# Performance work log

Hardware: AMD Instinct MI355X
Metric: run time of the kernel (lower is better)

The kernel has to match this reference:

```python
import jax, jax.numpy as jnp
import numpy as np

F = 128; K = 64; SR_CUT = 10.0
NB = 5; NRI = 3; NRA = 2; NRO = 1
N_ATOMS = 10000; N_PAIRS = 320000


def act(x):
    # shifted softplus: softplus(x) - log(2)
    return jax.nn.softplus(x) - jnp.log(2.0).astype(x.dtype)


def residual(x, W1, b1, W2, b2):
    # PhysNet residual: x + dense2(dense1(act(x))) with activation on dense1
    h = act(act(x) @ W1 + b1)
    return x + h @ W2 + b2


def cutoff_fn(D):
    x = D / SR_CUT
    x3 = x * x * x; x4 = x3 * x; x5 = x4 * x
    return jnp.where(x < 1.0, 1.0 - 6.0 * x5 + 15.0 * x4 - 10.0 * x3, 0.0)


def setup_inputs() -> dict:
    key = jax.random.key(0)
    ks = jax.random.split(key, 24)

    def nrm(k, shape, s=0.05):
        return (jax.random.normal(k, shape) * s).astype(jnp.float32)

    inp = {}
    inp["Z"] = jax.random.randint(ks[0], (N_ATOMS,), 1, 95)
    inp["R"] = (jax.random.normal(ks[1], (N_ATOMS, 3)) * 3.0).astype(jnp.float32)
    inp["idx_i"] = jax.random.randint(ks[2], (N_PAIRS,), 0, N_ATOMS)
    inp["idx_j"] = jax.random.randint(ks[3], (N_PAIRS,), 0, N_ATOMS)
    s3 = float(np.sqrt(3.0))
    inp["embeddings"] = jax.random.uniform(ks[4], (95, F), minval=-s3, maxval=s3).astype(jnp.float32)
    inp["rbf_centers"] = jnp.linspace(1.0, float(np.exp(-SR_CUT)), K).astype(jnp.float32)
    width = (0.5 / ((1.0 - float(np.exp(-SR_CUT))) / K)) ** 2
    inp["rbf_widths"] = jnp.full((K,), width, dtype=jnp.float32)
    inp["k2f_W"] = nrm(ks[5], (NB, K, F))
    inp["Wi"] = nrm(ks[6], (NB, F, F)); inp["bi"] = jnp.zeros((NB, F), jnp.float32)
    inp["Wj"] = nrm(ks[7], (NB, F, F)); inp["bj"] = jnp.zeros((NB, F), jnp.float32)
    inp["ri_W1"] = nrm(ks[8], (NB, NRI, F, F)); inp["ri_b1"] = jnp.zeros((NB, NRI, F), jnp.float32)
    inp["ri_W2"] = nrm(ks[9], (NB, NRI, F, F)); inp["ri_b2"] = jnp.zeros((NB, NRI, F), jnp.float32)
    inp["dW"] = nrm(ks[10], (NB, F, F)); inp["db"] = jnp.zeros((NB, F), jnp.float32)
    inp["u"] = jnp.ones((NB, F), jnp.float32)
    inp["ra_W1"] = nrm(ks[11], (NB, NRA, F, F)); inp["ra_b1"] = jnp.zeros((NB, NRA, F), jnp.float32)
    inp["ra_W2"] = nrm(ks[12], (NB, NRA, F, F)); inp["ra_b2"] = jnp.zeros((NB, NRA, F), jnp.float32)
    inp["ro_W1"] = nrm(ks[13], (NB, NRO, F, F)); inp["ro_b1"] = jnp.zeros((NB, NRO, F), jnp.float32)
    inp["ro_W2"] = nrm(ks[14], (NB, NRO, F, F)); inp["ro_b2"] = jnp.zeros((NB, NRO, F), jnp.float32)
    inp["out_W"] = nrm(ks[15], (NB, F, 2))
    inp["Escale"] = jnp.ones((95,), jnp.float32); inp["Eshift"] = jnp.zeros((95,), jnp.float32)
    inp["Qscale"] = jnp.ones((95,), jnp.float32); inp["Qshift"] = jnp.zeros((95,), jnp.float32)
    return inp


def reference(Z, R, idx_i, idx_j, embeddings, rbf_centers, rbf_widths, k2f_W, Wi, bi, Wj, bj,
              ri_W1, ri_b1, ri_W2, ri_b2, dW, db, u, ra_W1, ra_b1, ra_W2, ra_b2,
              ro_W1, ro_b1, ro_W2, ro_b2, out_W, Escale, Eshift, Qscale, Qshift):
    N = R.shape[0]
    # gather-based interatomic distances: gather -> sub -> sumsq -> relu -> sqrt
    dR = R[idx_i] - R[idx_j]                                   # [P,3]
    Dij = jnp.sqrt(jax.nn.relu(jnp.sum(dR * dR, axis=-1)))     # [P]
    # RBF expansion with smooth cutoff
    rbf = cutoff_fn(Dij)[:, None] * jnp.exp(-rbf_widths * (jnp.exp(-Dij)[:, None] - rbf_centers) ** 2)  # [P,K]
    x = embeddings[Z]                                          # [N,F]
    Ea = jnp.zeros((N,), x.dtype)
    Qa = jnp.zeros((N,), x.dtype)
    nhloss = jnp.zeros((), x.dtype)
    last2 = None
    for b in range(NB):
        # --- interaction layer ---
        g = rbf @ k2f_W[b]                                     # [P,F]
        xa = act(x)
        xi = act(xa @ Wi[b] + bi[b])                           # [N,F]
        xj_feat = act(xa @ Wj[b] + bj[b])                      # [N,F]
        msg = g * xj_feat[idx_j]                               # [P,F] gather + modulate
        m = xi + jax.ops.segment_sum(msg, idx_i, num_segments=N)
        for l in range(NRI):
            m = residual(m, ri_W1[b, l], ri_b1[b, l], ri_W2[b, l], ri_b2[b, l])
        m = act(m)
        x = u[b] * x + m @ dW[b] + db[b]
        for l in range(NRA):
            x = residual(x, ra_W1[b, l], ra_b1[b, l], ra_W2[b, l], ra_b2[b, l])
        # --- output block ---
        o = x
        for l in range(NRO):
            o = residual(o, ro_W1[b, l], ro_b1[b, l], ro_W2[b, l], ro_b2[b, l])
        out = act(o) @ out_W[b]                                # [N,2] -> (Ea, Qa)
        Ea = Ea + out[:, 0]
        Qa = Qa + out[:, 1]
        out2 = out * out
        if b > 0:
            nhloss = nhloss + jnp.mean(out2 / (out2 + last2 + 1e-7))
        last2 = out2
    Ea = Escale[Z] * Ea + Eshift[Z]
    Qa = Qscale[Z] * Qa + Qshift[Z]
    return Ea, Qa, Dij, nhloss
```

## Files before the change

### kernel.cpp

```cpp
#include <hip/hip_runtime.h>

typedef __attribute__((ext_vector_type(8))) short bfrag;
typedef __attribute__((ext_vector_type(4))) float ffrag;

__device__ __forceinline__ unsigned short f2b(float f){
  unsigned int u = __float_as_uint(f);
  return (unsigned short)((u + 0x7FFFu + ((u >> 16) & 1u)) >> 16);
}
__device__ __forceinline__ float b2f_lo(unsigned int v){
  return __uint_as_float(v << 16);
}
__device__ __forceinline__ float b2f_hi(unsigned int v){
  return __uint_as_float(v & 0xFFFF0000u);
}
__device__ __forceinline__ float actf(float v){
  float e = __builtin_amdgcn_exp2f(-fabsf(v)*1.44269504088896341f);
  return fmaxf(v, 0.f) + __builtin_amdgcn_logf(1.f + e)*0.69314718055994531f - 0.69314718055994531f;
}

__global__ __launch_bounds__(256) void k_zero(float* p, int n){
  int i = blockIdx.x*256 + threadIdx.x;
  if (i < n) p[i] = 0.f;
}

__global__ __launch_bounds__(256) void k_dij_count(
    const float* __restrict__ R, const int* __restrict__ idx_i, const int* __restrict__ idx_j,
    float* __restrict__ DijF, float* __restrict__ Dout, int* __restrict__ counts, int P){
  int p = blockIdx.x*256 + threadIdx.x;
  if (p >= P) return;
  int i = idx_i[p], j = idx_j[p];
  float dx = R[i*3+0] - R[j*3+0];
  float dy = R[i*3+1] - R[j*3+1];
  float dz = R[i*3+2] - R[j*3+2];
  float D = sqrtf(fmaxf(dx*dx + dy*dy + dz*dz, 0.f));
  DijF[p] = D;
  Dout[p] = D;
  atomicAdd(&counts[i], 1);
}

__global__ __launch_bounds__(1024) void k_scan(const int* __restrict__ counts,
    int* __restrict__ cursor, int N){
  __shared__ int wsum[16];
  int tid = threadIdx.x;
  int CH = (N + 1023) >> 10;
  int base = tid * CH;
  int s = 0;
  for (int i = 0; i < CH; ++i){
    int idx = base + i;
    s += (idx < N) ? counts[idx] : 0;
  }
  int lane = tid & 63, w = tid >> 6;
  int v = s;
  #pragma unroll
  for (int off = 1; off < 64; off <<= 1){
    int t = __shfl_up(v, off, 64);
    if (lane >= off) v += t;
  }
  if (lane == 63) wsum[w] = v;
  __syncthreads();
  if (tid < 16){
    int t = wsum[tid];
    int vv = t;
    #pragma unroll
    for (int off = 1; off < 16; off <<= 1){
      int u = __shfl_up(vv, off, 64);
      if (tid >= off) vv += u;
    }
    wsum[tid] = vv - t;
  }
  __syncthreads();
  int run = (v - s) + wsum[w];
  for (int i = 0; i < CH; ++i){
    int idx = base + i;
    if (idx < N){ cursor[idx] = run; run += counts[idx]; }
  }
}

__global__ __launch_bounds__(256) void k_scatter(const int* __restrict__ idx_i,
    const int* __restrict__ idx_j, const float* __restrict__ DijF,
    int* __restrict__ cursor, int* __restrict__ i_s, int* __restrict__ j_s,
    float* __restrict__ D_s, int P){
  int p = blockIdx.x*256 + threadIdx.x;
  if (p >= P) return;
  int i = idx_i[p];
  int pos = atomicAdd(&cursor[i], 1);
  i_s[pos] = i;
  j_s[pos] = idx_j[p];
  D_s[pos] = DijF[p];
}

__global__ __launch_bounds__(256) void k_rbf(
    const float* __restrict__ D_s, const float* __restrict__ cent, const float* __restrict__ wid,
    unsigned short* __restrict__ rbf_s, int P){
  int gid = blockIdx.x*256 + threadIdx.x;
  if (gid >= P*8) return;
  int t = gid >> 3, kg = gid & 7;
  float D = D_s[t];
  float xc = D * 0.1f;
  float cut = 0.f;
  if (xc < 1.f){
    float x3 = xc*xc*xc, x4 = x3*xc, x5 = x4*xc;
    cut = 1.f - 6.f*x5 + 15.f*x4 - 10.f*x3;
  }
  float eD = __builtin_amdgcn_exp2f(-D*1.44269504088896341f);
  bfrag o;
  #pragma unroll
  for (int i = 0; i < 8; ++i){
    int k = kg*8 + i;
    float tt = eD - cent[k];
    float v = cut * __builtin_amdgcn_exp2f(-wid[k]*tt*tt*1.44269504088896341f);
    o[i] = (short)f2b(v);
  }
  *(bfrag*)(rbf_s + (size_t)gid*8) = o;
}

__global__ __launch_bounds__(256) void k_prepAll(
    const float* __restrict__ riW1, const float* __restrict__ riW2,
    const float* __restrict__ dW,   const float* __restrict__ raW1,
    const float* __restrict__ raW2, const float* __restrict__ roW1,
    const float* __restrict__ roW2, const float* __restrict__ Wi,
    const float* __restrict__ Wj,   const float* __restrict__ k2f,
    const float* __restrict__ outW,
    unsigned short* __restrict__ WBall, unsigned short* __restrict__ k2fP,
    unsigned short* __restrict__ outWB){
  int gid = blockIdx.x*256 + threadIdx.x;
  if (gid < 75*2048){
    int i = gid >> 11, r = gid & 2047;
    const float* S;
    int slot;
    if (i < 15)      { S = riW1 + (size_t)i*16384;      slot = (i/3)*15 + 2*(i%3); }
    else if (i < 30) { int j=i-15; S = riW2 + (size_t)j*16384; slot = (j/3)*15 + 2*(j%3) + 1; }
    else if (i < 35) { int j=i-30; S = dW   + (size_t)j*16384; slot = j*15 + 6; }
    else if (i < 45) { int j=i-35; S = raW1 + (size_t)j*16384; slot = (j/2)*15 + 7 + 2*(j%2); }
    else if (i < 55) { int j=i-45; S = raW2 + (size_t)j*16384; slot = (j/2)*15 + 8 + 2*(j%2); }
    else if (i < 60) { int j=i-55; S = roW1 + (size_t)j*16384; slot = j*15 + 11; }
    else if (i < 65) { int j=i-60; S = roW2 + (size_t)j*16384; slot = j*15 + 12; }
    else if (i < 70) { int j=i-65; S = Wi   + (size_t)j*16384; slot = ((j==0)?4:(j-1))*15 + 13; }
    else             { int j=i-70; S = Wj   + (size_t)j*16384; slot = ((j==0)?4:(j-1))*15 + 14; }
    int fr = r >> 6, l = r & 63;
    int T = fr >> 2, k0 = fr & 3;
    int n = T*16 + (l & 15);
    int kbase = k0*32 + (l >> 4)*8;
    unsigned short* D = WBall + ((size_t)slot*2048 + r)*8;
    ushort4 o0, o1;
    o0.x=f2b(S[(kbase+0)*128+n]); o0.y=f2b(S[(kbase+1)*128+n]);
    o0.z=f2b(S[(kbase+2)*128+n]); o0.w=f2b(S[(kbase+3)*128+n]);
    o1.x=f2b(S[(kbase+4)*128+n]); o1.y=f2b(S[(kbase+5)*128+n]);
    o1.z=f2b(S[(kbase+6)*128+n]); o1.w=f2b(S[(kbase+7)*128+n]);
    ((ushort4*)D)[0]=o0; ((ushort4*)D)[1]=o1;
  } else if (gid < 75*2048 + 5120){
    int g = gid - 75*2048;
    int l = g & 63, fr = (g >> 6) & 15, b = g >> 10;
    int tile = fr >> 1, kh = fr & 1;
    const float* src = k2f + (size_t)b*64*128;
    int n = tile*16 + (l & 15);
    int kbase = kh*32 + (l >> 4)*8;
    ushort4 o0, o1;
    o0.x = f2b(src[(kbase+0)*128+n]); o0.y = f2b(src[(kbase+1)*128+n]);
    o0.z = f2b(src[(kbase+2)*128+n]); o0.w = f2b(src[(kbase+3)*128+n]);
    o1.x = f2b(src[(kbase+4)*128+n]); o1.y = f2b(src[(kbase+5)*128+n]);
    o1.z = f2b(src[(kbase+6)*128+n]); o1.w = f2b(src[(kbase+7)*128+n]);
    ushort4* dst = (ushort4*)(k2fP + (size_t)g*8);
    dst[0] = o0; dst[1] = o1;
  } else if (gid < 75*2048 + 5120 + 1280){
    int g = gid - (75*2048 + 5120);
    int b = g >> 8, r = g & 255;
    int l = r & 63;
    int col = l & 15;
    int k0 = r >> 6;
    int kbase = k0*32 + (l >> 4)*8;
    ushort4 o0 = {0,0,0,0}, o1 = {0,0,0,0};
    if (col < 2){
      const float* S = outW + (size_t)b*256;
      o0.x=f2b(S[(kbase+0)*2+col]); o0.y=f2b(S[(kbase+1)*2+col]);
      o0.z=f2b(S[(kbase+2)*2+col]); o0.w=f2b(S[(kbase+3)*2+col]);
      o1.x=f2b(S[(kbase+4)*2+col]); o1.y=f2b(S[(kbase+5)*2+col]);
      o1.z=f2b(S[(kbase+6)*2+col]); o1.w=f2b(S[(kbase+7)*2+col]);
    }
    unsigned short* D = outWB + ((size_t)b*256 + r)*8;
    ((ushort4*)D)[0]=o0; ((ushort4*)D)[1]=o1;
  }
}

__device__ __forceinline__ void mmtile(const unsigned short* tile,
    const unsigned short* __restrict__ WB, int w, int l, ffrag C[4]){
  int m = l & 15, q = l >> 4;
  bfrag A[4];
  #pragma unroll
  for (int k0 = 0; k0 < 4; ++k0)
    A[k0] = *(const bfrag*)(tile + m*136 + k0*32 + q*8);
  #pragma unroll
  for (int tt = 0; tt < 4; ++tt){
    ffrag c = {0.f,0.f,0.f,0.f};
    const bfrag* bp = (const bfrag*)(WB + (((w*4+tt)*4)*64 + l)*8);
    #pragma unroll
    for (int k0 = 0; k0 < 4; ++k0)
      c = __builtin_amdgcn_mfma_f32_16x16x32_bf16(A[k0], bp[k0*64], c, 0, 0, 0);
    C[tt] = c;
  }
}

__global__ __launch_bounds__(128) void k_phase1m(
    const int* __restrict__ Z, const float* __restrict__ emb,
    const unsigned short* __restrict__ WB45,
    const float* __restrict__ bi0, const float* __restrict__ bj0,
    float* __restrict__ x_g, float* __restrict__ m_g, unsigned short* __restrict__ xjb_g, int N){
  __shared__ unsigned short tile[16*136];
  int tid = threadIdx.x, w = tid >> 6, l = tid & 63;
  int m = l & 15, q = l >> 4, rbase = blockIdx.x*16;
  #pragma unroll
  for (int r = 0; r < 4; ++r){
    int row = rbase + q*4 + r;
    int z = Z[row];
    #pragma unroll
    for (int tt = 0; tt < 4; ++tt){
      int c = (w*4+tt)*16 + m;
      float v = emb[(size_t)z*128 + c];
      x_g[(size_t)row*128 + c] = v;
      tile[(q*4+r)*136 + c] = f2b(actf(v));
    }
  }
  __syncthreads();
  ffrag C[4];
  mmtile(tile, WB45 + 13*16384, w, l, C);
  #pragma unroll
  for (int tt = 0; tt < 4; ++tt){
    int c = (w*4+tt)*16 + m;
    float bb = bi0[c];
    #pragma unroll
    for (int r = 0; r < 4; ++r)
      m_g[(size_t)(rbase + q*4 + r)*128 + c] = actf(C[tt][r] + bb);
  }
  mmtile(tile, WB45 + 14*16384, w, l, C);
  #pragma unroll
  for (int tt = 0; tt < 4; ++tt){
    int c = (w*4+tt)*16 + m;
    float bb = bj0[c];
    #pragma unroll
    for (int r = 0; r < 4; ++r)
      xjb_g[(size_t)(rbase + q*4 + r)*128 + c] = f2b(actf(C[tt][r] + bb));
  }
}

__global__ __launch_bounds__(256) void k_pairmsg2(
    const unsigned short* __restrict__ rbf_s, const unsigned short* __restrict__ k2fP,
    const int* __restrict__ i_s, const int* __restrict__ j_s,
    const unsigned short* __restrict__ xj, float* __restrict__ m_g, int P){
  __shared__ float G[4][16*130];
  int tid = threadIdx.x, w = tid >> 6, l = tid & 63;
  float* Gw = &G[w][0];
  bfrag B[16];
  #pragma unroll
  for (int t = 0; t < 8; ++t){
    #pragma unroll
    for (int kh = 0; kh < 2; ++kh)
      B[t*2+kh] = *(const bfrag*)(k2fP + (size_t)((t*2+kh)*64 + l)*8);
  }
  int wstart = (blockIdx.x*4 + w)*128;
  if (wstart >= P) return;
  int row16 = l & 15, quad = l >> 4;
  float a0 = 0.f, a1 = 0.f;
  int iCur = -1;
  bfrag A0 = *(const bfrag*)(rbf_s + (size_t)(wstart + row16)*64 + quad*8);
  bfrag A1 = *(const bfrag*)(rbf_s + (size_t)(wstart + row16)*64 + 32 + quad*8);
  int4 iv[4], jv[4];
  #pragma unroll
  for (int g = 0; g < 4; ++g){
    iv[g] = *(const int4*)(i_s + wstart + g*4);
    jv[g] = *(const int4*)(j_s + wstart + g*4);
  }
  unsigned int xv[16];
  {
    const int* jp = (const int*)jv;
    #pragma unroll
    for (int k = 0; k < 16; ++k)
      xv[k] = *(const unsigned int*)(xj + (size_t)jp[k]*128 + 2*l);
  }
  #pragma unroll 1
  for (int bi2 = 0; bi2 < 8; ++bi2){
    int bt = wstart + bi2*16;
    const int* ip = (const int*)iv;
    int4 niv[4], njv[4];
    if (bi2 < 7){
      int btn = bt + 16;
      #pragma unroll
      for (int g = 0; g < 4; ++g){
        niv[g] = *(const int4*)(i_s + btn + g*4);
        njv[g] = *(const int4*)(j_s + btn + g*4);
      }
    }
    #pragma unroll
    for (int t = 0; t < 8; ++t){
      ffrag C = {0.f,0.f,0.f,0.f};
      C = __builtin_amdgcn_mfma_f32_16x16x32_bf16(A0, B[t*2],   C, 0, 0, 0);
      C = __builtin_amdgcn_mfma_f32_16x16x32_bf16(A1, B[t*2+1], C, 0, 0, 0);
      #pragma unroll
      for (int r = 0; r < 4; ++r)
        Gw[(quad*4+r)*130 + t*16 + row16] = C[r];
    }
    bfrag nA0, nA1;
    unsigned int nxv[16];
    if (bi2 < 7){
      int btn = bt + 16;
      nA0 = *(const bfrag*)(rbf_s + (size_t)(btn + row16)*64 + quad*8);
      nA1 = *(const bfrag*)(rbf_s + (size_t)(btn + row16)*64 + 32 + quad*8);
      const int* njp = (const int*)njv;
      #pragma unroll
      for (int k = 0; k < 16; ++k)
        nxv[k] = *(const unsigned int*)(xj + (size_t)njp[k]*128 + 2*l);
    }
    #pragma unroll
    for (int k = 0; k < 16; ++k){
      int i = ip[k];
      if (i != iCur){
        if (iCur >= 0){
          unsafeAtomicAdd(&m_g[(size_t)iCur*128 + 2*l],     a0);
          unsafeAtomicAdd(&m_g[(size_t)iCur*128 + 2*l + 1], a1);
        }
        iCur = i; a0 = 0.f; a1 = 0.f;
      }
      float g0 = Gw[k*130 + 2*l], g1 = Gw[k*130 + 2*l + 1];
      a0 = fmaf(g0, b2f_lo(xv[k]), a0);
      a1 = fmaf(g1, b2f_hi(xv[k]), a1);
    }
    if (bi2 < 7){
      A0 = nA0; A1 = nA1;
      #pragma unroll
      for (int g = 0; g < 4; ++g){ iv[g] = niv[g]; jv[g] = njv[g]; }
      #pragma unroll
      for (int k = 0; k < 16; ++k) xv[k] = nxv[k];
    }
  }
  if (iCur >= 0){
    unsafeAtomicAdd(&m_g[(size_t)iCur*128 + 2*l],     a0);
    unsafeAtomicAdd(&m_g[(size_t)iCur*128 + 2*l + 1], a1);
  }
}

template<int HASNEXT, int NH>
__global__ __launch_bounds__(512) void k_phase2m(
    float* __restrict__ m_g, float* __restrict__ x_g, unsigned short* __restrict__ xjb_g,
    const unsigned short* __restrict__ WBb,
    const float* __restrict__ rib1, const float* __restrict__ rib2,
    const float* __restrict__ db, const float* __restrict__ u,
    const float* __restrict__ rab1, const float* __restrict__ rab2,
    const float* __restrict__ rob1, const float* __restrict__ rob2,
    const float* __restrict__ biN, const float* __restrict__ bjN,
    const unsigned short* __restrict__ outWBb,
    float* __restrict__ Ea, float* __restrict__ Qa,
    float* __restrict__ last2, float* __restrict__ nh, int N){
  __shared__ unsigned short tiles[2][2][16*136];
  __shared__ float biasS[16*128];
  int tid = threadIdx.x, w = tid >> 6, l = tid & 63;
  int m = l & 15, q = l >> 4, rbase = blockIdx.x*32;
  int c = w*16 + m;
  ffrag mC[2], xC[2], C[2];
  float xrow[2][4];
  int cur = 0;
  const int nst = HASNEXT ? 15 : 13;
  const int slotSeq[15] = {0,1,2,3,4,5,6,7,8,9,10,
                           HASNEXT?13:11, HASNEXT?14:12, 11, 12};
  bfrag Bb[2][4];
  #pragma unroll
  for (int k0 = 0; k0 < 4; ++k0)
    Bb[0][k0] = *(const bfrag*)(WBb + (size_t)slotSeq[0]*16384 + (size_t)((w*4+k0)*64 + l)*8);

  if (tid < 128){
    biasS[0*128+tid]  = rib1[tid];
    biasS[1*128+tid]  = rib1[128+tid];
    biasS[2*128+tid]  = rib1[256+tid];
    biasS[3*128+tid]  = rib2[tid];
    biasS[4*128+tid]  = rib2[128+tid];
    biasS[5*128+tid]  = rib2[256+tid];
    biasS[6*128+tid]  = db[tid];
    biasS[7*128+tid]  = u[tid];
    biasS[8*128+tid]  = rab1[tid];
    biasS[9*128+tid]  = rab1[128+tid];
    biasS[10*128+tid] = rab2[tid];
    biasS[11*128+tid] = rab2[128+tid];
    biasS[12*128+tid] = rob1[tid];
    biasS[13*128+tid] = rob2[tid];
    biasS[14*128+tid] = biN[tid];
    biasS[15*128+tid] = bjN[tid];
  }
  #pragma unroll
  for (int h = 0; h < 2; ++h){
    #pragma unroll
    for (int r = 0; r < 4; ++r){
      int row = rbase + h*16 + q*4 + r;
      int rs = row < N ? row : N-1;
      xrow[h][r] = x_g[(size_t)rs*128 + c];
      float v = m_g[(size_t)rs*128 + c];
      mC[h][r] = v;
      tiles[h][0][(q*4+r)*136 + c] = f2b(actf(v));
    }
  }
  #pragma unroll 2
  for (int s = 0; s < nst; ++s){
    __syncthreads();
    if (s+1 < nst){
      #pragma unroll
      for (int k0 = 0; k0 < 4; ++k0)
        Bb[(s+1)&1][k0] = *(const bfrag*)(WBb + (size_t)slotSeq[s+1]*16384 + (size_t)((w*4+k0)*64 + l)*8);
    }
    #pragma unroll
    for (int h = 0; h < 2; ++h){
      const unsigned short* tp = &tiles[h][cur][0];
      ffrag cc = {0.f,0.f,0.f,0.f};
      #pragma unroll
      for (int k0 = 0; k0 < 4; ++k0){
        bfrag A = *(const bfrag*)(tp + m*136 + k0*32 + q*8);
        cc = __builtin_amdgcn_mfma_f32_16x16x32_bf16(A, Bb[s&1][k0], cc, 0, 0, 0);
      }
      C[h] = cc;
    }
    if (HASNEXT && s == 11){
      float bb = biasS[14*128 + c];
      #pragma unroll
      for (int h = 0; h < 2; ++h)
        #pragma unroll
        for (int r = 0; r < 4; ++r){
          int row = rbase + h*16 + q*4 + r;
          if (row < N) m_g[(size_t)row*128 + c] = actf(C[h][r] + bb);
        }
    } else if (HASNEXT && s == 12){
      float bb = biasS[15*128 + c];
      #pragma unroll
      for (int h = 0; h < 2; ++h)
        #pragma unroll
        for (int r = 0; r < 4; ++r){
          int row = rbase + h*16 + q*4 + r;
          if (row < N) xjb_g[(size_t)row*128 + c] = f2b(actf(C[h][r] + bb));
        }
    } else if (s == 6){
      float uu = biasS[7*128 + c], bb = biasS[6*128 + c];
      #pragma unroll
      for (int h = 0; h < 2; ++h)
        #pragma unroll
        for (int r = 0; r < 4; ++r){
          float nv = uu*xrow[h][r] + C[h][r] + bb;
          xC[h][r] = nv;
          tiles[h][1-cur][(q*4+r)*136 + c] = f2b(actf(nv));
        }
      cur ^= 1;
    } else if (s == 1 || s == 3 || s == 5){
      float bb = biasS[(3 + (s>>1))*128 + c];
      #pragma unroll
      for (int h = 0; h < 2; ++h)
        #pragma unroll
        for (int r = 0; r < 4; ++r){
          float nv = mC[h][r] + C[h][r] + bb;
          mC[h][r] = nv;
          tiles[h][1-cur][(q*4+r)*136 + c] = f2b(actf(nv));
        }
      cur ^= 1;
    } else if (s == 8 || s == 10){
      float bb = biasS[(10 + ((s-8)>>1))*128 + c];
      #pragma unroll
      for (int h = 0; h < 2; ++h)
        #pragma unroll
        for (int r = 0; r < 4; ++r){
          float nv = xC[h][r] + C[h][r] + bb;
          xC[h][r] = nv;
          tiles[h][1-cur][(q*4+r)*136 + c] = f2b(actf(nv));
          if (HASNEXT && s == 10){
            int row = rbase + h*16 + q*4 + r;
            if (row < N) x_g[(size_t)row*128 + c] = nv;
          }
        }
      cur ^= 1;
    } else if ((HASNEXT && s == 14) || (!HASNEXT && s == 12)){
      float bb = biasS[13*128 + c];
      #pragma unroll
      for (int h = 0; h < 2; ++h)
        #pragma unroll
        for (int r = 0; r < 4; ++r){
          float ov = xC[h][r] + C[h][r] + bb;
          tiles[h][1-cur][(q*4+r)*136 + c] = f2b(actf(ov));
        }
      cur ^= 1;
    } else {
      int bidx = (s==0)?0:(s==2)?1:(s==4)?2:(s==7)?8:(s==9)?9:12;
      float bb = biasS[bidx*128 + c];
      #pragma unroll
      for (int h = 0; h < 2; ++h)
        #pragma unroll
        for (int r = 0; r < 4; ++r)
          tiles[h][1-cur][(q*4+r)*136 + c] = f2b(actf(C[h][r] + bb));
      cur ^= 1;
    }
  }
  __syncthreads();
  if (w < 2){
    const unsigned short* tp = &tiles[w][cur][0];
    bfrag A[4];
    #pragma unroll
    for (int k0 = 0; k0 < 4; ++k0)
      A[k0] = *(const bfrag*)(tp + m*136 + k0*32 + q*8);
    ffrag Ch = {0.f,0.f,0.f,0.f};
    #pragma unroll
    for (int k0 = 0; k0 < 4; ++k0){
      bfrag B = *(const bfrag*)(outWBb + (size_t)(k0*64 + l)*8);
      Ch = __builtin_amdgcn_mfma_f32_16x16x32_bf16(A[k0], B, Ch, 0, 0, 0);
    }
    int col = m;
    if (col < 2){
      float tpa = 0.f;
      #pragma unroll
      for (int r = 0; r < 4; ++r){
        int row = rbase + w*16 + q*4 + r;
        if (row < N){
          float val = Ch[r];
          if (NH){
            if (col == 0) Ea[row] += val; else Qa[row] += val;
          } else {
            if (col == 0) Ea[row]  = val; else Qa[row]  = val;
          }
          float sq = val*val;
          if (NH){
            float lastv = last2[row*2 + col];
            tpa += sq/(sq + lastv + 1e-7f);
          }
          last2[row*2 + col] = sq;
        }
      }
      if (NH) unsafeAtomicAdd(nh, tpa);
    }
  }
}

__global__ __launch_bounds__(256) void k_final(
    const int* __restrict__ Z, const float* __restrict__ Ea, const float* __restrict__ Qa,
    const float* __restrict__ Es, const float* __restrict__ Eh,
    const float* __restrict__ Qs, const float* __restrict__ Qh,
    const float* __restrict__ nh, float* __restrict__ out, int N, int P){
  int n = blockIdx.x*256 + threadIdx.x;
  if (n < N){
    int z = Z[n];
    out[n]   = Es[z]*Ea[n] + Eh[z];
    out[N+n] = Qs[z]*Qa[n] + Qh[z];
  }
  if (blockIdx.x == 0 && threadIdx.x == 0)
    out[(size_t)2*N + P] = nh[0] / (2.f * (float)N);
}

extern "C" void kernel_launch(void* const* d_in, const int* in_sizes, int n_in,
                              void* d_out, int out_size, void* d_ws, size_t ws_size,
                              hipStream_t stream){
  const int N = in_sizes[0];
  const int P = in_sizes[2];
  const int F = 128;

  const int* Z      = (const int*)d_in[0];
  const float* R    = (const float*)d_in[1];
  const int* idx_i  = (const int*)d_in[2];
  const int* idx_j  = (const int*)d_in[3];
  const float* emb  = (const float*)d_in[4];
  const float* cent = (const float*)d_in[5];
  const float* wid  = (const float*)d_in[6];
  const float* k2f  = (const float*)d_in[7];
  const float* Wi   = (const float*)d_in[8];  const float* bi   = (const float*)d_in[9];
  const float* Wj   = (const float*)d_in[10]; const float* bj   = (const float*)d_in[11];
  const float* riW1 = (const float*)d_in[12]; const float* rib1 = (const float*)d_in[13];
  const float* riW2 = (const float*)d_in[14]; const float* rib2 = (const float*)d_in[15];
  const float* dWp  = (const float*)d_in[16]; const float* dbp  = (const float*)d_in[17];
  const float* u    = (const float*)d_in[18];
  const float* raW1 = (const float*)d_in[19]; const float* rab1 = (const float*)d_in[20];
  const float* raW2 = (const float*)d_in[21]; const float* rab2 = (const float*)d_in[22];
  const float* roW1 = (const float*)d_in[23]; const float* rob1 = (const float*)d_in[24];
  const float* roW2 = (const float*)d_in[25]; const float* rob2 = (const float*)d_in[26];
  const float* outW = (const float*)d_in[27];
  const float* Es   = (const float*)d_in[28]; const float* Eh   = (const float*)d_in[29];
  const float* Qs   = (const float*)d_in[30]; const float* Qh   = (const float*)d_in[31];

  char* ws = (char*)d_ws;
  size_t off = 0;
  float* DijF  = (float*)(ws + off); off += (size_t)P*4;
  float* D_s   = (float*)(ws + off); off += (size_t)P*4;
  int*   i_s   = (int*)  (ws + off); off += (size_t)P*4;
  int*   j_s   = (int*)  (ws + off); off += (size_t)P*4;
  unsigned short* rbf_s = (unsigned short*)(ws + off); off += (size_t)P*64*2;
  unsigned short* k2fP  = (unsigned short*)(ws + off); off += (size_t)5*16*64*8*2;
  unsigned short* WBall = (unsigned short*)(ws + off); off += (size_t)75*16384*2;
  unsigned short* outWB = (unsigned short*)(ws + off); off += (size_t)5*2048*2;
  float* x     = (float*)(ws + off); off += (size_t)N*F*4;
  unsigned short* xjb = (unsigned short*)(ws + off); off += (size_t)N*F*2;
  float* m     = (float*)(ws + off); off += (size_t)N*F*4;
  float* last2 = (float*)(ws + off); off += (size_t)N*2*4;
  float* Ea    = (float*)(ws + off); off += (size_t)N*4;
  float* Qa    = (float*)(ws + off); off += (size_t)N*4;
  float* nh    = (float*)(ws + off); off += 256;
  int*   counts= (int*)  (ws + off); off += (size_t)N*4;
  int*   cursor= (int*)  (ws + off); off += (size_t)N*4;

  float* outF = (float*)d_out;
  float* Dout = outF + (size_t)2*N;

  const int nzero = N + 64;
  k_zero<<<dim3((nzero+255)/256), dim3(256), 0, stream>>>(nh, nzero);
  k_dij_count<<<dim3((P+255)/256), dim3(256), 0, stream>>>(R, idx_i, idx_j, DijF, Dout, counts, P);
  k_scan<<<dim3(1), dim3(1024), 0, stream>>>(counts, cursor, N);
  k_scatter<<<dim3((P+255)/256), dim3(256), 0, stream>>>(idx_i, idx_j, DijF, cursor, i_s, j_s, D_s, P);
  k_rbf<<<dim3((P*8+255)/256), dim3(256), 0, stream>>>(D_s, cent, wid, rbf_s, P);
  k_prepAll<<<dim3((75*2048 + 5120 + 1280 + 255)/256), dim3(256), 0, stream>>>(
      riW1, riW2, dWp, raW1, raW2, roW1, roW2, Wi, Wj, k2f, outW, WBall, k2fP, outWB);

  const int G16 = (N + 15)/16;
  k_phase1m<<<dim3(G16), dim3(128), 0, stream>>>(Z, emb, WBall + (size_t)4*15*16384,
                                                 bi, bj, x, m, xjb, N);

  const int pmg = (P + 511)/512;
  const int G32 = (N + 31)/32;
  for (int b = 0; b < 5; ++b){
    k_pairmsg2<<<dim3(pmg), dim3(256), 0, stream>>>(rbf_s, k2fP + (size_t)b*16*64*8,
                                                    i_s, j_s, xjb, m, P);
    const unsigned short* WBb = WBall + (size_t)b*15*16384;
    const float* a_rib1 = rib1 + (size_t)b*3*F;
    const float* a_rib2 = rib2 + (size_t)b*3*F;
    const float* a_db   = dbp  + (size_t)b*F;
    const float* a_u    = u    + (size_t)b*F;
    const float* a_rab1 = rab1 + (size_t)b*2*F;
    const float* a_rab2 = rab2 + (size_t)b*2*F;
    const float* a_rob1 = rob1 + (size_t)b*F;
    const float* a_rob2 = rob2 + (size_t)b*F;
    int bn = (b < 4) ? (b+1) : 0;
    const float* a_biN = bi + (size_t)bn*F;
    const float* a_bjN = bj + (size_t)bn*F;
    const unsigned short* oWB = outWB + (size_t)b*2048;
    if (b == 0){
      k_phase2m<1,0><<<dim3(G32), dim3(512), 0, stream>>>(m, x, xjb, WBb,
        a_rib1, a_rib2, a_db, a_u, a_rab1, a_rab2, a_rob1, a_rob2,
        a_biN, a_bjN, oWB, Ea, Qa, last2, nh, N);
    } else if (b < 4){
      k_phase2m<1,1><<<dim3(G32), dim3(512), 0, stream>>>(m, x, xjb, WBb,
        a_rib1, a_rib2, a_db, a_u, a_rab1, a_rab2, a_rob1, a_rob2,
        a_biN, a_bjN, oWB, Ea, Qa, last2, nh, N);
    } else {
      k_phase2m<0,1><<<dim3(G32), dim3(512), 0, stream>>>(m, x, xjb, WBb,
        a_rib1, a_rib2, a_db, a_u, a_rab1, a_rab2, a_rob1, a_rob2,
        a_biN, a_bjN, oWB, Ea, Qa, last2, nh, N);
    }
  }
  k_final<<<dim3((N+255)/256), dim3(256), 0, stream>>>(Z, Ea, Qa, Es, Eh, Qs, Qh, nh, outF, N, P);
}
```

Before: 493.1 us.

## Fuse RBF expansion into pair-message kernel and reduce per atom block in LDS

Removes the separate RBF kernel and its P×64 bf16 buffer, recomputing the radial basis on the fly from sorted distances inside the pair-message kernel for each of the five blocks. The pair-message kernel is re-partitioned so each workgroup owns 16 destination atoms, using cursor (end offsets after scatter) to find its pair range. Contributions are accumulated with LDS atomics and written back with one vector add per row instead of global float atomics. This trades global memory traffic and atomics for repeated exp computation, plus tiles shared by neighbouring atom groups being processed twice.

```diff
diff --git a/kernel.cpp b/kernel.cpp
--- a/kernel.cpp
+++ b/kernel.cpp
@@ -16,6 +16,24 @@
 __device__ __forceinline__ float actf(float v){
   float e = __builtin_amdgcn_exp2f(-fabsf(v)*1.44269504088896341f);
   return fmaxf(v, 0.f) + __builtin_amdgcn_logf(1.f + e)*0.69314718055994531f - 0.69314718055994531f;
+}
+
+__device__ __forceinline__ void mkA(float D, const float* __restrict__ centL,
+    const float* __restrict__ widL, int quad, bfrag& A0, bfrag& A1){
+  float xc = D * 0.1f;
+  float cut = 0.f;
+  if (xc < 1.f){
+    float x3 = xc*xc*xc, x4 = x3*xc, x5 = x4*xc;
+    cut = 1.f - 6.f*x5 + 15.f*x4 - 10.f*x3;
+  }
+  float eD = __builtin_amdgcn_exp2f(-D*1.44269504088896341f);
+  #pragma unroll
+  for (int i = 0; i < 8; ++i){
+    float t0 = eD - centL[quad*8+i];
+    A0[i] = (short)f2b(cut*__builtin_amdgcn_exp2f(-widL[quad*8+i]*t0*t0*1.44269504088896341f));
+    float t1 = eD - centL[32+quad*8+i];
+    A1[i] = (short)f2b(cut*__builtin_amdgcn_exp2f(-widL[32+quad*8+i]*t1*t1*1.44269504088896341f));
+  }
 }
 
 __global__ __launch_bounds__(256) void k_zero(float* p, int n){
@@ -87,31 +105,6 @@
   i_s[pos] = i;
   j_s[pos] = idx_j[p];
   D_s[pos] = DijF[p];
-}
-
-__global__ __launch_bounds__(256) void k_rbf(
-    const float* __restrict__ D_s, const float* __restrict__ cent, const float* __restrict__ wid,
-    unsigned short* __restrict__ rbf_s, int P){
-  int gid = blockIdx.x*256 + threadIdx.x;
-  if (gid >= P*8) return;
-  int t = gid >> 3, kg = gid & 7;
-  float D = D_s[t];
-  float xc = D * 0.1f;
-  float cut = 0.f;
-  if (xc < 1.f){
-    float x3 = xc*xc*xc, x4 = x3*xc, x5 = x4*xc;
-    cut = 1.f - 6.f*x5 + 15.f*x4 - 10.f*x3;
-  }
-  float eD = __builtin_amdgcn_exp2f(-D*1.44269504088896341f);
-  bfrag o;
-  #pragma unroll
-  for (int i = 0; i < 8; ++i){
-    int k = kg*8 + i;
-    float tt = eD - cent[k];
-    float v = cut * __builtin_amdgcn_exp2f(-wid[k]*tt*tt*1.44269504088896341f);
-    o[i] = (short)f2b(v);
-  }
-  *(bfrag*)(rbf_s + (size_t)gid*8) = o;
 }
 
 __global__ __launch_bounds__(256) void k_prepAll(
@@ -242,12 +235,20 @@
   }
 }
 
-__global__ __launch_bounds__(256) void k_pairmsg2(
-    const unsigned short* __restrict__ rbf_s, const unsigned short* __restrict__ k2fP,
+__global__ __launch_bounds__(256, 3) void k_pairmsg3(
+    const float* __restrict__ D_s, const float* __restrict__ cent, const float* __restrict__ wid,
+    const unsigned short* __restrict__ k2fP,
     const int* __restrict__ i_s, const int* __restrict__ j_s,
-    const unsigned short* __restrict__ xj, float* __restrict__ m_g, int P){
+    const int* __restrict__ ends,
+    const unsigned short* __restrict__ xj, float* __restrict__ m_g, int N, int P){
   __shared__ float G[4][16*130];
+  __shared__ float mL[16*128];
+  __shared__ float centL[64], widL[64];
   int tid = threadIdx.x, w = tid >> 6, l = tid & 63;
+  int rbase = blockIdx.x*16;
+  if (tid < 64){ centL[tid] = cent[tid]; widL[tid] = wid[tid]; }
+  #pragma unroll
+  for (int i = 0; i < 8; ++i) mL[i*256 + tid] = 0.f;
   float* Gw = &G[w][0];
   bfrag B[16];
   #pragma unroll
@@ -256,84 +257,105 @@
     for (int kh = 0; kh < 2; ++kh)
       B[t*2+kh] = *(const bfrag*)(k2fP + (size_t)((t*2+kh)*64 + l)*8);
   }
-  int wstart = (blockIdx.x*4 + w)*128;
-  if (wstart >= P) return;
+  int pstart = (rbase == 0) ? 0 : ends[rbase-1];
+  int rlast  = (rbase+15 < N) ? rbase+15 : N-1;
+  int pend   = ends[rlast];
   int row16 = l & 15, quad = l >> 4;
+  __syncthreads();
   float a0 = 0.f, a1 = 0.f;
   int iCur = -1;
-  bfrag A0 = *(const bfrag*)(rbf_s + (size_t)(wstart + row16)*64 + quad*8);
-  bfrag A1 = *(const bfrag*)(rbf_s + (size_t)(wstart + row16)*64 + 32 + quad*8);
-  int4 iv[4], jv[4];
-  #pragma unroll
-  for (int g = 0; g < 4; ++g){
-    iv[g] = *(const int4*)(i_s + wstart + g*4);
-    jv[g] = *(const int4*)(j_s + wstart + g*4);
-  }
-  unsigned int xv[16];
-  {
-    const int* jp = (const int*)jv;
-    #pragma unroll
-    for (int k = 0; k < 16; ++k)
-      xv[k] = *(const unsigned int*)(xj + (size_t)jp[k]*128 + 2*l);
-  }
-  #pragma unroll 1
-  for (int bi2 = 0; bi2 < 8; ++bi2){
-    int bt = wstart + bi2*16;
-    const int* ip = (const int*)iv;
-    int4 niv[4], njv[4];
-    if (bi2 < 7){
-      int btn = bt + 16;
-      #pragma unroll
-      for (int g = 0; g < 4; ++g){
-        niv[g] = *(const int4*)(i_s + btn + g*4);
-        njv[g] = *(const int4*)(j_s + btn + g*4);
+  int b0 = pstart >> 4, b1 = (pend + 15) >> 4;
+  int bt = b0 + w;
+  if (bt < b1){
+    int base = bt << 4;
+    int4 iv[4], jv[4];
+    #pragma unroll
+    for (int g = 0; g < 4; ++g){
+      iv[g] = *(const int4*)(i_s + base + g*4);
+      jv[g] = *(const int4*)(j_s + base + g*4);
+    }
+    bfrag A0, A1;
+    { float D0 = D_s[base + row16]; mkA(D0, centL, widL, quad, A0, A1); }
+    unsigned int xv[16];
+    {
+      const int* jp = (const int*)jv;
+      #pragma unroll
+      for (int k = 0; k < 16; ++k)
+        xv[k] = *(const unsigned int*)(xj + (size_t)jp[k]*128 + 2*l);
+    }
+    #pragma unroll 1
+    for (; bt < b1; bt += 4){
+      int btn = bt + 4;
+      bool more = btn < b1;
+      int basen = btn << 4;
+      int4 niv[4], njv[4];
+      float nD = 0.f;
+      if (more){
+        #pragma unroll
+        for (int g = 0; g < 4; ++g){
+          niv[g] = *(const int4*)(i_s + basen + g*4);
+          njv[g] = *(const int4*)(j_s + basen + g*4);
+        }
+        nD = D_s[basen + row16];
       }
-    }
-    #pragma unroll
-    for (int t = 0; t < 8; ++t){
-      ffrag C = {0.f,0.f,0.f,0.f};
-      C = __builtin_amdgcn_mfma_f32_16x16x32_bf16(A0, B[t*2],   C, 0, 0, 0);
-      C = __builtin_amdgcn_mfma_f32_16x16x32_bf16(A1, B[t*2+1], C, 0, 0, 0);
-      #pragma unroll
-      for (int r = 0; r < 4; ++r)
-        Gw[(quad*4+r)*130 + t*16 + row16] = C[r];
-    }
-    bfrag nA0, nA1;
-    unsigned int nxv[16];
-    if (bi2 < 7){
-      int btn = bt + 16;
-      nA0 = *(const bfrag*)(rbf_s + (size_t)(btn + row16)*64 + quad*8);
-      nA1 = *(const bfrag*)(rbf_s + (size_t)(btn + row16)*64 + 32 + quad*8);
-      const int* njp = (const int*)njv;
-      #pragma unroll
-      for (int k = 0; k < 16; ++k)
-        nxv[k] = *(const unsigned int*)(xj + (size_t)njp[k]*128 + 2*l);
-    }
-    #pragma unroll
-    for (int k = 0; k < 16; ++k){
-      int i = ip[k];
-      if (i != iCur){
-        if (iCur >= 0){
-          unsafeAtomicAdd(&m_g[(size_t)iCur*128 + 2*l],     a0);
-          unsafeAtomicAdd(&m_g[(size_t)iCur*128 + 2*l + 1], a1);
-        }
-        iCur = i; a0 = 0.f; a1 = 0.f;
+      #pragma unroll
+      for (int t = 0; t < 8; ++t){
+        ffrag C = {0.f,0.f,0.f,0.f};
+        C = __builtin_amdgcn_mfma_f32_16x16x32_bf16(A0, B[t*2],   C, 0, 0, 0);
+        C = __builtin_amdgcn_mfma_f32_16x16x32_bf16(A1, B[t*2+1], C, 0, 0, 0);
+        #pragma unroll
+        for (int r = 0; r < 4; ++r)
+          Gw[(quad*4+r)*130 + t*16 + row16] = C[r];
       }
-      float g0 = Gw[k*130 + 2*l], g1 = Gw[k*130 + 2*l + 1];
-      a0 = fmaf(g0, b2f_lo(xv[k]), a0);
-      a1 = fmaf(g1, b2f_hi(xv[k]), a1);
-    }
-    if (bi2 < 7){
-      A0 = nA0; A1 = nA1;
-      #pragma unroll
-      for (int g = 0; g < 4; ++g){ iv[g] = niv[g]; jv[g] = njv[g]; }
-      #pragma unroll
-      for (int k = 0; k < 16; ++k) xv[k] = nxv[k];
+      bfrag nA0, nA1;
+      unsigned int nxv[16];
+      if (more){
+        mkA(nD, centL, widL, quad, nA0, nA1);
+        const int* njp = (const int*)njv;
+        #pragma unroll
+        for (int k = 0; k < 16; ++k)
+          nxv[k] = *(const unsigned int*)(xj + (size_t)njp[k]*128 + 2*l);
+      }
+      const int* ip = (const int*)iv;
+      #pragma unroll
+      for (int k = 0; k < 16; ++k){
+        int i = ip[k];
+        if ((unsigned)(i - rbase) < 16u){
+          if (i != iCur){
+            if (iCur >= 0){
+              atomicAdd(&mL[(iCur-rbase)*128 + 2*l],     a0);
+              atomicAdd(&mL[(iCur-rbase)*128 + 2*l + 1], a1);
+            }
+            iCur = i; a0 = 0.f; a1 = 0.f;
+          }
+          float g0 = Gw[k*130 + 2*l], g1 = Gw[k*130 + 2*l + 1];
+          a0 = fmaf(g0, b2f_lo(xv[k]), a0);
+          a1 = fmaf(g1, b2f_hi(xv[k]), a1);
+        }
+      }
+      if (more){
+        A0 = nA0; A1 = nA1;
+        #pragma unroll
+        for (int g = 0; g < 4; ++g){ iv[g] = niv[g]; jv[g] = njv[g]; }
+        #pragma unroll
+        for (int k = 0; k < 16; ++k) xv[k] = nxv[k];
+      }
     }
   }
   if (iCur >= 0){
-    unsafeAtomicAdd(&m_g[(size_t)iCur*128 + 2*l],     a0);
-    unsafeAtomicAdd(&m_g[(size_t)iCur*128 + 2*l + 1], a1);
+    atomicAdd(&mL[(iCur-rbase)*128 + 2*l],     a0);
+    atomicAdd(&mL[(iCur-rbase)*128 + 2*l + 1], a1);
+  }
+  __syncthreads();
+  int row = tid >> 4;
+  if (rbase + row < N){
+    float* mp = m_g + (size_t)(rbase + row)*128 + (tid & 15)*8;
+    const float* sp = &mL[row*128 + (tid & 15)*8];
+    float4 v0 = *(float4*)mp, v1 = *(float4*)(mp + 4);
+    float4 s0 = *(const float4*)sp, s1 = *(const float4*)(sp + 4);
+    v0.x += s0.x; v0.y += s0.y; v0.z += s0.z; v0.w += s0.w;
+    v1.x += s1.x; v1.y += s1.y; v1.z += s1.z; v1.w += s1.w;
+    *(float4*)mp = v0; *(float4*)(mp + 4) = v1;
   }
 }
 
@@ -579,7 +601,6 @@
   float* D_s   = (float*)(ws + off); off += (size_t)P*4;
   int*   i_s   = (int*)  (ws + off); off += (size_t)P*4;
   int*   j_s   = (int*)  (ws + off); off += (size_t)P*4;
-  unsigned short* rbf_s = (unsigned short*)(ws + off); off += (size_t)P*64*2;
   unsigned short* k2fP  = (unsigned short*)(ws + off); off += (size_t)5*16*64*8*2;
   unsigned short* WBall = (unsigned short*)(ws + off); off += (size_t)75*16384*2;
   unsigned short* outWB = (unsigned short*)(ws + off); off += (size_t)5*2048*2;
@@ -601,7 +622,6 @@
   k_dij_count<<<dim3((P+255)/256), dim3(256), 0, stream>>>(R, idx_i, idx_j, DijF, Dout, counts, P);
   k_scan<<<dim3(1), dim3(1024), 0, stream>>>(counts, cursor, N);
   k_scatter<<<dim3((P+255)/256), dim3(256), 0, stream>>>(idx_i, idx_j, DijF, cursor, i_s, j_s, D_s, P);
-  k_rbf<<<dim3((P*8+255)/256), dim3(256), 0, stream>>>(D_s, cent, wid, rbf_s, P);
   k_prepAll<<<dim3((75*2048 + 5120 + 1280 + 255)/256), dim3(256), 0, stream>>>(
       riW1, riW2, dWp, raW1, raW2, roW1, roW2, Wi, Wj, k2f, outW, WBall, k2fP, outWB);
 
@@ -609,11 +629,11 @@
   k_phase1m<<<dim3(G16), dim3(128), 0, stream>>>(Z, emb, WBall + (size_t)4*15*16384,
                                                  bi, bj, x, m, xjb, N);
 
-  const int pmg = (P + 511)/512;
   const int G32 = (N + 31)/32;
   for (int b = 0; b < 5; ++b){
-    k_pairmsg2<<<dim3(pmg), dim3(256), 0, stream>>>(rbf_s, k2fP + (size_t)b*16*64*8,
-                                                    i_s, j_s, xjb, m, P);
+    k_pairmsg3<<<dim3(G16), dim3(256), 0, stream>>>(D_s, cent, wid,
+                                                    k2fP + (size_t)b*16*64*8,
+                                                    i_s, j_s, cursor, xjb, m, N, P);
     const unsigned short* WBb = WBall + (size_t)b*15*16384;
     const float* a_rib1 = rib1 + (size_t)b*3*F;
     const float* a_rib2 = rib2 + (size_t)b*3*F;
```

Measured after the change: 732.9 us. 48.6% more time.

## Drop software prefetch in pair-message kernel, halve per-wave work, raise occupancy

Applied to the files above, without the earlier changes.

The pair-message kernel no longer double-buffers the next 16-pair batch's indices, RBF fragments and gathered features in registers. Each wave now handles 64 pairs instead of 128, so the grid doubles. A launch-bounds hint asks for 3 blocks per SM, and readfirstlane keeps the pair indices scalar. The aim is to cut register pressure so more waves hide the gather latency, at the cost of losing explicit prefetch and issuing more atomic flushes at the wave boundaries.

```diff
diff --git a/kernel.cpp b/kernel.cpp
--- a/kernel.cpp
+++ b/kernel.cpp
@@ -13,6 +13,7 @@
 __device__ __forceinline__ float b2f_hi(unsigned int v){
   return __uint_as_float(v & 0xFFFF0000u);
 }
+__device__ __forceinline__ int rfl(int v){ return __builtin_amdgcn_readfirstlane(v); }
 __device__ __forceinline__ float actf(float v){
   float e = __builtin_amdgcn_exp2f(-fabsf(v)*1.44269504088896341f);
   return fmaxf(v, 0.f) + __builtin_amdgcn_logf(1.f + e)*0.69314718055994531f - 0.69314718055994531f;
@@ -242,7 +243,7 @@
   }
 }
 
-__global__ __launch_bounds__(256) void k_pairmsg2(
+__global__ __launch_bounds__(256, 3) void k_pairmsg2(
     const unsigned short* __restrict__ rbf_s, const unsigned short* __restrict__ k2fP,
     const int* __restrict__ i_s, const int* __restrict__ j_s,
     const unsigned short* __restrict__ xj, float* __restrict__ m_g, int P){
@@ -251,44 +252,30 @@
   float* Gw = &G[w][0];
   bfrag B[16];
   #pragma unroll
-  for (int t = 0; t < 8; ++t){
-    #pragma unroll
-    for (int kh = 0; kh < 2; ++kh)
-      B[t*2+kh] = *(const bfrag*)(k2fP + (size_t)((t*2+kh)*64 + l)*8);
-  }
-  int wstart = (blockIdx.x*4 + w)*128;
+  for (int t = 0; t < 16; ++t)
+    B[t] = *(const bfrag*)(k2fP + (size_t)(t*64 + l)*8);
+  int wstart = (blockIdx.x*4 + w)*64;
   if (wstart >= P) return;
   int row16 = l & 15, quad = l >> 4;
   float a0 = 0.f, a1 = 0.f;
   int iCur = -1;
-  bfrag A0 = *(const bfrag*)(rbf_s + (size_t)(wstart + row16)*64 + quad*8);
-  bfrag A1 = *(const bfrag*)(rbf_s + (size_t)(wstart + row16)*64 + 32 + quad*8);
-  int4 iv[4], jv[4];
-  #pragma unroll
-  for (int g = 0; g < 4; ++g){
-    iv[g] = *(const int4*)(i_s + wstart + g*4);
-    jv[g] = *(const int4*)(j_s + wstart + g*4);
-  }
-  unsigned int xv[16];
-  {
-    const int* jp = (const int*)jv;
+  #pragma unroll 1
+  for (int bi2 = 0; bi2 < 4; ++bi2){
+    int bt = wstart + bi2*16;
+    bfrag A0 = *(const bfrag*)(rbf_s + (size_t)(bt + row16)*64 + quad*8);
+    bfrag A1 = *(const bfrag*)(rbf_s + (size_t)(bt + row16)*64 + 32 + quad*8);
+    int ip[16], jp[16];
+    #pragma unroll
+    for (int g = 0; g < 4; ++g){
+      int4 it = *(const int4*)(i_s + bt + g*4);
+      int4 jt = *(const int4*)(j_s + bt + g*4);
+      ip[g*4+0]=rfl(it.x); ip[g*4+1]=rfl(it.y); ip[g*4+2]=rfl(it.z); ip[g*4+3]=rfl(it.w);
+      jp[g*4+0]=rfl(jt.x); jp[g*4+1]=rfl(jt.y); jp[g*4+2]=rfl(jt.z); jp[g*4+3]=rfl(jt.w);
+    }
+    unsigned int xv[16];
     #pragma unroll
     for (int k = 0; k < 16; ++k)
       xv[k] = *(const unsigned int*)(xj + (size_t)jp[k]*128 + 2*l);
-  }
-  #pragma unroll 1
-  for (int bi2 = 0; bi2 < 8; ++bi2){
-    int bt = wstart + bi2*16;
-    const int* ip = (const int*)iv;
-    int4 niv[4], njv[4];
-    if (bi2 < 7){
-      int btn = bt + 16;
-      #pragma unroll
-      for (int g = 0; g < 4; ++g){
-        niv[g] = *(const int4*)(i_s + btn + g*4);
-        njv[g] = *(const int4*)(j_s + btn + g*4);
-      }
-    }
     #pragma unroll
     for (int t = 0; t < 8; ++t){
       ffrag C = {0.f,0.f,0.f,0.f};
@@ -297,17 +284,6 @@
       #pragma unroll
       for (int r = 0; r < 4; ++r)
         Gw[(quad*4+r)*130 + t*16 + row16] = C[r];
-    }
-    bfrag nA0, nA1;
-    unsigned int nxv[16];
-    if (bi2 < 7){
-      int btn = bt + 16;
-      nA0 = *(const bfrag*)(rbf_s + (size_t)(btn + row16)*64 + quad*8);
-      nA1 = *(const bfrag*)(rbf_s + (size_t)(btn + row16)*64 + 32 + quad*8);
-      const int* njp = (const int*)njv;
-      #pragma unroll
-      for (int k = 0; k < 16; ++k)
-        nxv[k] = *(const unsigned int*)(xj + (size_t)njp[k]*128 + 2*l);
     }
     #pragma unroll
     for (int k = 0; k < 16; ++k){
@@ -322,13 +298,6 @@
       float g0 = Gw[k*130 + 2*l], g1 = Gw[k*130 + 2*l + 1];
       a0 = fmaf(g0, b2f_lo(xv[k]), a0);
       a1 = fmaf(g1, b2f_hi(xv[k]), a1);
-    }
-    if (bi2 < 7){
-      A0 = nA0; A1 = nA1;
-      #pragma unroll
-      for (int g = 0; g < 4; ++g){ iv[g] = niv[g]; jv[g] = njv[g]; }
-      #pragma unroll
-      for (int k = 0; k < 16; ++k) xv[k] = nxv[k];
     }
   }
   if (iCur >= 0){
@@ -609,7 +578,7 @@
   k_phase1m<<<dim3(G16), dim3(128), 0, stream>>>(Z, emb, WBall + (size_t)4*15*16384,
                                                  bi, bj, x, m, xjb, N);
 
-  const int pmg = (P + 511)/512;
+  const int pmg = (P + 255)/256;
   const int G32 = (N + 31)/32;
   for (int b = 0; b < 5; ++b){
     k_pairmsg2<<<dim3(pmg), dim3(256), 0, stream>>>(rbf_s, k2fP + (size_t)b*16*64*8,
```

Measured after the change: 447.7 us. 9.2% less time.
